# Performance work log

Measured on AMD Instinct MI355X. Metric: run time of the kernel, lower is better.

The kernel has to match this reference:

```python
import jax, jax.numpy as jnp
import numpy as np

B, V = 2048, 64          # batch of polygons, vertices per polygon
D = 2 * V                # data_dim (flattened 2D coords)
HID, TDIM, NL = 256, 128, 4
NH_HID, FPH = 4, 64      # hidden heads, per-head features (hidden_dim//4)
NIN = 2 + 4 + TDIM       # coords + pos_enc(4) + time emb


def _gat_layer(h, src, tgt, W, a_src, a_tgt, b, skip, concat, act, N):
    # gordicaleksa pytorch-GAT GATLayer (imp3), dropout=0
    NH, FOUT = a_src.shape
    proj = (h @ W).reshape(N, NH, FOUT)                       # (N,NH,FOUT)
    s_src = (proj * a_src).sum(-1)                            # (N,NH)
    s_tgt = (proj * a_tgt).sum(-1)
    e = jax.nn.leaky_relu(s_src[src] + s_tgt[tgt], negative_slope=0.2)  # (E,NH)
    m = jax.ops.segment_max(e, tgt, num_segments=N)           # stable segment softmax
    ex = jnp.exp(e - m[tgt])
    denom = jax.ops.segment_sum(ex, tgt, num_segments=N)
    alpha = ex / (denom[tgt] + 1e-16)                         # (E,NH)
    out = jax.ops.segment_sum(proj[src] * alpha[:, :, None], tgt, num_segments=N)
    if skip is None:                                          # FIN == FOUT -> direct residual
        out = out + h[:, None, :]
    else:
        out = out + (h @ skip).reshape(N, NH, FOUT)
    out = out.reshape(N, NH * FOUT) if concat else out.mean(axis=1)
    out = out + b
    return jax.nn.elu(out) if act else out


def _forward(x, t, tW, tb, layers, h1W, h1b, h2W, h2b):
    Bsz, Dd = x.shape
    Vn = Dd // 2
    N = Bsz * Vn
    coords = x.reshape(N, 2)
    graph_index = jnp.repeat(jnp.arange(Bsz), Vn)
    node_index = jnp.tile(jnp.arange(Vn), Bsz)
    # SinusoidalPosEmb(TDIM) + Linear + SiLU
    half = TDIM // 2
    freqs = jnp.exp(-jnp.log(10000.0) * jnp.arange(half, dtype=jnp.float32) / (half - 1))
    te = t.astype(jnp.float32)[:, None] * freqs[None, :]
    temb = jnp.concatenate([jnp.sin(te), jnp.cos(te)], axis=1)
    temb = jax.nn.silu(temb @ tW + tb)
    # cycle positional features
    phase = node_index.astype(jnp.float32) * (2.0 * jnp.pi / Vn)
    pos = jnp.stack([jnp.sin(phase), jnp.cos(phase), jnp.sin(2.0 * phase), jnp.cos(2.0 * phase)], axis=1)
    h = jnp.concatenate([coords, pos, temb[graph_index]], axis=1)  # (N, NIN)
    # cycle edge_index: src=[self,self,self], tgt=[next,prev,self]
    base = graph_index * Vn
    slf = jnp.arange(N)
    nxt = base + jnp.remainder(node_index + 1, Vn)
    prv = base + jnp.remainder(node_index - 1, Vn)
    src = jnp.concatenate([slf, slf, slf])
    tgt = jnp.concatenate([nxt, prv, slf])
    for i, (W, a_s, a_t, b, skip) in enumerate(layers):
        last = (i == len(layers) - 1)
        h = _gat_layer(h, src, tgt, W, a_s, a_t, b, skip, concat=not last, act=not last, N=N)
    h = jax.nn.silu(h @ h1W + h1b)
    noise = h @ h2W + h2b                                     # (N, 2)
    return noise.reshape(Bsz, Dd)


def setup_inputs() -> dict:
    key = jax.random.key(0)
    ks = iter(jax.random.split(key, 48))
    def nrm(shape, s=0.05):
        return (jax.random.normal(next(ks), shape, jnp.float32) * s)
    inp = {}
    inp["x"] = jax.random.normal(next(ks), (B, D), jnp.float32)
    inp["t"] = jax.random.randint(next(ks), (B,), 0, 1000)
    inp["tW"] = nrm((TDIM, TDIM)); inp["tb"] = jnp.zeros((TDIM,), jnp.float32)
    fins = [NIN, NH_HID * FPH, NH_HID * FPH, NH_HID * FPH]
    fouts = [FPH, FPH, FPH, HID]
    nhs = [NH_HID, NH_HID, NH_HID, 1]
    for i in range(NL):
        inp[f"W{i}"] = nrm((fins[i], nhs[i] * fouts[i]))
        inp[f"asrc{i}"] = nrm((nhs[i], fouts[i]))
        inp[f"atgt{i}"] = nrm((nhs[i], fouts[i]))
        inp[f"b{i}"] = jnp.zeros((nhs[i] * fouts[i] if i < NL - 1 else fouts[i],), jnp.float32)
    for i in range(NL - 1):  # last layer: FIN==FOUT -> identity skip
        inp[f"skip{i}"] = nrm((fins[i], nhs[i] * fouts[i]))
    inp["h1W"] = nrm((HID, HID)); inp["h1b"] = jnp.zeros((HID,), jnp.float32)
    inp["h2W"] = nrm((HID, 2)); inp["h2b"] = jnp.zeros((2,), jnp.float32)
    return inp


def reference(x, t, tW, tb,
              W0, asrc0, atgt0, b0, skip0,
              W1, asrc1, atgt1, b1, skip1,
              W2, asrc2, atgt2, b2, skip2,
              W3, asrc3, atgt3, b3,
              h1W, h1b, h2W, h2b):
    layers = [(W0, asrc0, atgt0, b0, skip0),
              (W1, asrc1, atgt1, b1, skip1),
              (W2, asrc2, atgt2, b2, skip2),
              (W3, asrc3, atgt3, b3, None)]
    return _forward(x, t, tW, tb, layers, h1W, h1b, h2W, h2b)
```

## Files before the change

### kernel.cpp

```cpp
#include <hip/hip_runtime.h>
#include <hip/hip_bf16.h>

#define VN    64
#define KPAD  264

typedef __bf16 bf16x8 __attribute__((ext_vector_type(8)));
typedef __bf16 bf16x4 __attribute__((ext_vector_type(4)));
typedef float  f32x4  __attribute__((ext_vector_type(4)));

__device__ __forceinline__ float fexp(float x) { return __expf(x); }
__device__ __forceinline__ float frcp(float x) { return __builtin_amdgcn_rcpf(x); }

#define OFF_W0   0
#define OFF_SK0  40960
#define OFF_W1   81920
#define OFF_SK1  147456
#define OFF_W2   212992
#define OFF_SK2  278528
#define OFF_W3   344064
#define OFF_H1W  409600
#define OFF_SA0  475136
#define OFF_SA1  477696
#define OFF_SA2  481792
#define OFF_SA3  485888
#define OFF_END  489984

__global__ void setup_all(const float* __restrict__ W0s, const float* __restrict__ sk0s,
                          const float* __restrict__ W1s, const float* __restrict__ sk1s,
                          const float* __restrict__ W2s, const float* __restrict__ sk2s,
                          const float* __restrict__ W3s, const float* __restrict__ h1Ws,
                          const float* __restrict__ h2W,
                          const float* __restrict__ as0, const float* __restrict__ at0,
                          const float* __restrict__ as1, const float* __restrict__ at1,
                          const float* __restrict__ as2, const float* __restrict__ at2,
                          const float* __restrict__ as3, const float* __restrict__ at3,
                          const int* __restrict__ t, const float* __restrict__ tW,
                          const float* __restrict__ tb,
                          float* __restrict__ h2wt, float* __restrict__ d_temb,
                          __bf16* __restrict__ wp)
{
  int blk = blockIdx.x, tid = threadIdx.x;
  if (blk < 116) {
    __shared__ float shw[16][257];
    const float* src; int fin, dstoff, s;
    if (blk < 20) {
      if (blk < 10) { src = W0s;  dstoff = OFF_W0;  s = blk; }
      else          { src = sk0s; dstoff = OFF_SK0; s = blk - 10; }
      fin = 134;
    } else {
      int r = (blk - 20) >> 4;
      s = (blk - 20) & 15;
      const float* srcs[6] = {W1s, sk1s, W2s, sk2s, W3s, h1Ws};
      const int    offs[6] = {OFF_W1, OFF_SK1, OFF_W2, OFF_SK2, OFF_W3, OFF_H1W};
      src = srcs[r]; dstoff = offs[r]; fin = 256;
    }
#pragma unroll
    for (int it = 0; it < 16; it++) {
      int elem = it * 256 + tid;
      int r = elem >> 8, n = elem & 255;
      int k = s * 16 + r;
      shw[r][n] = (k < fin) ? src[k * 256 + n] : 0.0f;
    }
    __syncthreads();
#pragma unroll
    for (int it = 0; it < 16; it++) {
      int lin = it * 256 + tid;
      int k7 = lin & 7, n = (lin >> 3) & 255, cl = lin >> 11;
      wp[dstoff + s * 4096 + lin] = (__bf16)shw[cl * 8 + k7][n];
    }
  } else if (blk < 118) {
    int idx = (blk - 116) * 256 + tid;
    int c = idx >> 8, k = idx & 255;
    h2wt[idx] = h2W[k * 2 + c];
  } else if (blk < 176) {
    int idx = (blk - 118) * 256 + tid;
    if (idx < 14848) {
      int gk = idx >> 4, c = idx & 15;
      int li, k, fin, dstoff;
      if (gk < 160)      { li = 0; k = gk;       fin = 134; dstoff = OFF_SA0; }
      else if (gk < 416) { li = 1; k = gk - 160; fin = 256; dstoff = OFF_SA1; }
      else if (gk < 672) { li = 2; k = gk - 416; fin = 256; dstoff = OFF_SA2; }
      else               { li = 3; k = gk - 672; fin = 256; dstoff = OFF_SA3; }
      float v = 0.0f;
      if (k < fin) {
        if (li < 3) {
          if (c < 8) {
            int hd = c & 3;
            const float* Wm = (li == 0) ? W0s : (li == 1) ? W1s : W2s;
            const float* a  = (c < 4) ? ((li == 0) ? as0 : (li == 1) ? as1 : as2)
                                      : ((li == 0) ? at0 : (li == 1) ? at1 : at2);
            for (int f = 0; f < 64; f++)
              v += Wm[k * 256 + hd * 64 + f] * a[hd * 64 + f];
          }
        } else {
          if (c < 2) {
            const float* a = (c == 0) ? as3 : at3;
            for (int f = 0; f < 256; f++)
              v += W3s[k * 256 + f] * a[f];
          }
        }
      }
      wp[dstoff + ((k >> 3) * 16 + c) * 8 + (k & 7)] = (__bf16)v;
    }
  } else {
    __shared__ float se[2][128];
    int half = tid >> 7, tt = tid & 127;
    int b = (blk - 176) * 2 + half;
    int fi = tt & 63;
    float fr = expf(-logf(10000.0f) * (float)fi / 63.0f);
    float te = (float)t[b] * fr;
    se[half][tt] = (tt < 64) ? sinf(te) : cosf(te);
    __syncthreads();
    float a = tb[tt];
    for (int k = 0; k < 128; k++)
      a = fmaf(se[half][k], tW[k * 128 + tt], a);
    d_temb[b * 128 + tt] = a * frcp(1.0f + fexp(-a));
  }
}

template<int KS>
__device__ __forceinline__ void mfma_mm(const __bf16* __restrict__ Bp,
                                        f32x4 acc[4][4],
                                        const __bf16* __restrict__ shA,
                                        int l, int q, int colbase8)
{
#pragma unroll
  for (int s = 0; s < KS; s++) {
    bf16x8 af[4], bfr[4];
#pragma unroll
    for (int rt = 0; rt < 4; rt++)
      af[rt] = *(const bf16x8*)(shA + (rt * 16 + l) * KPAD + s * 32 + q * 8);
#pragma unroll
    for (int ct = 0; ct < 4; ct++)
      bfr[ct] = *(const bf16x8*)(Bp + (s * 4 + q) * 2048 + colbase8 + ct * 128);
#pragma unroll
    for (int rt = 0; rt < 4; rt++)
#pragma unroll
      for (int ct = 0; ct < 4; ct++)
        acc[rt][ct] = __builtin_amdgcn_mfma_f32_16x16x32_bf16(af[rt], bfr[ct], acc[rt][ct], 0, 0, 0);
  }
}

template<int KS>
__device__ __forceinline__ void mfma_mm_sc(const __bf16* __restrict__ Bp,
                                           const __bf16* __restrict__ SAp,
                                           f32x4 acc[4][4], f32x4 acc_sc[4],
                                           const __bf16* __restrict__ shA,
                                           int l, int q, int colbase8)
{
#pragma unroll
  for (int s = 0; s < KS; s++) {
    bf16x8 af[4], bfr[4], bsc;
#pragma unroll
    for (int rt = 0; rt < 4; rt++)
      af[rt] = *(const bf16x8*)(shA + (rt * 16 + l) * KPAD + s * 32 + q * 8);
#pragma unroll
    for (int ct = 0; ct < 4; ct++)
      bfr[ct] = *(const bf16x8*)(Bp + (s * 4 + q) * 2048 + colbase8 + ct * 128);
    bsc = *(const bf16x8*)(SAp + (s * 4 + q) * 128 + l * 8);
#pragma unroll
    for (int rt = 0; rt < 4; rt++) {
#pragma unroll
      for (int ct = 0; ct < 4; ct++)
        acc[rt][ct] = __builtin_amdgcn_mfma_f32_16x16x32_bf16(af[rt], bfr[ct], acc[rt][ct], 0, 0, 0);
      acc_sc[rt] = __builtin_amdgcn_mfma_f32_16x16x32_bf16(af[rt], bsc, acc_sc[rt], 0, 0, 0);
    }
  }
}

__global__ __launch_bounds__(256, 2)
void gat_poly_kernel(const float* __restrict__ x,
                     const float* __restrict__ b0, const float* __restrict__ b1,
                     const float* __restrict__ b2, const float* __restrict__ b3,
                     const float* __restrict__ h1b, const float* __restrict__ h2b,
                     const __bf16* __restrict__ WP,
                     const float* __restrict__ h2wt,
                     const float* __restrict__ d_temb,
                     float* __restrict__ out)
{
  __shared__ __bf16 bufA[VN * KPAD];
  __shared__ __bf16 bufB[VN * KPAD];
  __shared__ float  sh_temb[128];
  __shared__ float  sh_ssp[VN * 4];
  __shared__ float  sh_stp[VN * 4];
  __shared__ float  sh_al[VN][4][3];

  const int b    = blockIdx.x;
  const int tid  = threadIdx.x;
  const int w    = tid >> 6;
  const int lane = tid & 63;
  const int l    = lane & 15;
  const int q    = lane >> 4;
  const int cb   = w * 64;
  const int colbase8 = (cb + l) * 8;

  const int fq  = (tid & 63) * 4;
  const int ns  = (tid >> 6) * 16;
  const int qhd = fq >> 6;

  __bf16* hb = bufA;
  __bf16* ag = bufB;

  if (tid < 128) sh_temb[tid] = d_temb[b * 128 + tid];
  __syncthreads();

  for (int idx = tid; idx < VN * 160; idx += 256) {
    int n = idx / 160, k = idx - n * 160;
    float v = 0.0f;
    if (k < 2) {
      v = x[b * 128 + 2 * n + k];
    } else if (k < 6) {
      float ph  = (float)n * 0.09817477042468103f;
      float arg = (k < 4) ? ph : 2.0f * ph;
      v = ((k & 1) == 0) ? sinf(arg) : cosf(arg);
    } else if (k < 134) {
      v = sh_temb[k - 6];
    }
    hb[n * KPAD + k] = (__bf16)v;
  }
  __syncthreads();

  const int WOFFS[3]  = {OFF_W0, OFF_W1, OFF_W2};
  const int SOFFS[3]  = {OFF_SK0, OFF_SK1, OFF_SK2};
  const int SAOFFS[3] = {OFF_SA0, OFF_SA1, OFF_SA2};
  const float* Bs[3]  = {b0, b1, b2};

  for (int li = 0; li < 3; li++) {
    {
      f32x4 accS[4][4];
#pragma unroll
      for (int rt = 0; rt < 4; rt++)
#pragma unroll
        for (int ct = 0; ct < 4; ct++) accS[rt][ct] = (f32x4)0.0f;
      if (li == 0) mfma_mm<5>(WP + OFF_SK0,   accS, hb, l, q, colbase8);
      else         mfma_mm<8>(WP + SOFFS[li], accS, hb, l, q, colbase8);
      float b4[4];
#pragma unroll
      for (int ct = 0; ct < 4; ct++) b4[ct] = Bs[li][cb + ct * 16 + l];
#pragma unroll
      for (int rt = 0; rt < 4; rt++)
#pragma unroll
        for (int reg = 0; reg < 4; reg++) {
          int n = rt * 16 + q * 4 + reg;
#pragma unroll
          for (int ct = 0; ct < 4; ct++)
            ag[n * KPAD + cb + ct * 16 + l] = (__bf16)(accS[rt][ct][reg] + b4[ct]);
        }
    }

    f32x4 acc[4][4], acc_sc[4];
#pragma unroll
    for (int rt = 0; rt < 4; rt++) {
#pragma unroll
      for (int ct = 0; ct < 4; ct++) acc[rt][ct] = (f32x4)0.0f;
      acc_sc[rt] = (f32x4)0.0f;
    }
    if (li == 0) mfma_mm_sc<5>(WP + OFF_W0,    WP + OFF_SA0,    acc, acc_sc, hb, l, q, colbase8);
    else         mfma_mm_sc<8>(WP + WOFFS[li], WP + SAOFFS[li], acc, acc_sc, hb, l, q, colbase8);

    if (l < 8) {
#pragma unroll
      for (int rt = 0; rt < 4; rt++)
#pragma unroll
        for (int reg = 0; reg < 4; reg++) {
          int n = rt * 16 + q * 4 + reg;
          float v = acc_sc[rt][reg];
          if (l < 4) sh_ssp[n * 4 + l] = v;
          else       sh_stp[n * 4 + (l - 4)] = v;
        }
    }
    __syncthreads();

#pragma unroll
    for (int rt = 0; rt < 4; rt++)
#pragma unroll
      for (int reg = 0; reg < 4; reg++) {
        int n = rt * 16 + q * 4 + reg;
#pragma unroll
        for (int ct = 0; ct < 4; ct++)
          hb[n * KPAD + cb + ct * 16 + l] = (__bf16)acc[rt][ct][reg];
      }

    {
      int n = tid >> 2, hd = tid & 3;
      int prv = (n + 63) & 63, nxt = (n + 1) & 63;
      float stg = sh_stp[n * 4 + hd];
      float e0 = sh_ssp[prv * 4 + hd] + stg; e0 = (e0 < 0.0f) ? 0.2f * e0 : e0;
      float e1 = sh_ssp[nxt * 4 + hd] + stg; e1 = (e1 < 0.0f) ? 0.2f * e1 : e1;
      float e2 = sh_ssp[n * 4 + hd]   + stg; e2 = (e2 < 0.0f) ? 0.2f * e2 : e2;
      float mx = fmaxf(e0, fmaxf(e1, e2));
      float x0 = fexp(e0 - mx), x1 = fexp(e1 - mx), x2 = fexp(e2 - mx);
      float inv = frcp(x0 + x1 + x2 + 1e-16f);
      sh_al[n][hd][0] = x0 * inv;
      sh_al[n][hd][1] = x1 * inv;
      sh_al[n][hd][2] = x2 * inv;
    }
    __syncthreads();

    {
      float pm[4], pc[4];
      { bf16x4 v = *(const bf16x4*)(hb + ((ns + 63) & 63) * KPAD + fq);
#pragma unroll
        for (int j = 0; j < 4; j++) pm[j] = (float)v[j]; }
      { bf16x4 v = *(const bf16x4*)(hb + ns * KPAD + fq);
#pragma unroll
        for (int j = 0; j < 4; j++) pc[j] = (float)v[j]; }
#pragma unroll 4
      for (int i = 0; i < 16; i++) {
        int n = ns + i;
        bf16x4 pnv = *(const bf16x4*)(hb + ((n + 1) & 63) * KPAD + fq);
        bf16x4 agv = *(const bf16x4*)(ag + n * KPAD + fq);
        float a0 = sh_al[n][qhd][0], a1 = sh_al[n][qhd][1], a2 = sh_al[n][qhd][2];
        bf16x4 ov;
#pragma unroll
        for (int j = 0; j < 4; j++) {
          float pn = (float)pnv[j];
          float o = a0 * pm[j] + a1 * pn + a2 * pc[j] + (float)agv[j];
          o = (o > 0.0f) ? o : (fexp(o) - 1.0f);
          ov[j] = (__bf16)o;
          pm[j] = pc[j]; pc[j] = pn;
        }
        *(bf16x4*)(ag + n * KPAD + fq) = ov;
      }
    }
    __syncthreads();

    __bf16* tmp = hb; hb = ag; ag = tmp;
  }

  {
    f32x4 acc[4][4], acc_sc[4];
#pragma unroll
    for (int rt = 0; rt < 4; rt++) {
#pragma unroll
      for (int ct = 0; ct < 4; ct++) acc[rt][ct] = (f32x4)0.0f;
      acc_sc[rt] = (f32x4)0.0f;
    }
    mfma_mm_sc<8>(WP + OFF_W3, WP + OFF_SA3, acc, acc_sc, hb, l, q, colbase8);

    if (l < 2) {
#pragma unroll
      for (int rt = 0; rt < 4; rt++)
#pragma unroll
        for (int reg = 0; reg < 4; reg++) {
          int n = rt * 16 + q * 4 + reg;
          float v = acc_sc[rt][reg];
          if (l == 0) sh_ssp[n * 4] = v;
          else        sh_stp[n * 4] = v;
        }
    }
    __syncthreads();

#pragma unroll
    for (int rt = 0; rt < 4; rt++)
#pragma unroll
      for (int reg = 0; reg < 4; reg++) {
        int n = rt * 16 + q * 4 + reg;
#pragma unroll
        for (int ct = 0; ct < 4; ct++)
          ag[n * KPAD + cb + ct * 16 + l] = (__bf16)acc[rt][ct][reg];
      }

    if (tid < 64) {
      int n = tid;
      float ssn = sh_ssp[n * 4];
      float stn = sh_stp[n * 4];
      float ssp = __shfl(ssn, (n + 63) & 63, 64);
      float ssx = __shfl(ssn, (n + 1) & 63, 64);
      float e0 = ssp + stn; e0 = (e0 < 0.0f) ? 0.2f * e0 : e0;
      float e1 = ssx + stn; e1 = (e1 < 0.0f) ? 0.2f * e1 : e1;
      float e2 = ssn + stn; e2 = (e2 < 0.0f) ? 0.2f * e2 : e2;
      float mx = fmaxf(e0, fmaxf(e1, e2));
      float x0 = fexp(e0 - mx), x1 = fexp(e1 - mx), x2 = fexp(e2 - mx);
      float inv = frcp(x0 + x1 + x2 + 1e-16f);
      sh_al[n][0][0] = x0 * inv;
      sh_al[n][0][1] = x1 * inv;
      sh_al[n][0][2] = x2 * inv;
    }
    __syncthreads();

    {
      float b3r[4];
#pragma unroll
      for (int j = 0; j < 4; j++) b3r[j] = b3[fq + j];
      float pm[4], pc[4];
      { bf16x4 v = *(const bf16x4*)(ag + ((ns + 63) & 63) * KPAD + fq);
#pragma unroll
        for (int j = 0; j < 4; j++) pm[j] = (float)v[j]; }
      { bf16x4 v = *(const bf16x4*)(ag + ns * KPAD + fq);
#pragma unroll
        for (int j = 0; j < 4; j++) pc[j] = (float)v[j]; }
#pragma unroll 4
      for (int i = 0; i < 16; i++) {
        int n = ns + i;
        bf16x4 pnv = *(const bf16x4*)(ag + ((n + 1) & 63) * KPAD + fq);
        bf16x4 hrv = *(const bf16x4*)(hb + n * KPAD + fq);
        float a0 = sh_al[n][0][0], a1 = sh_al[n][0][1], a2 = sh_al[n][0][2];
        bf16x4 ov;
#pragma unroll
        for (int j = 0; j < 4; j++) {
          float pn = (float)pnv[j];
          float o = a0 * pm[j] + a1 * pn + a2 * pc[j] + (float)hrv[j] + b3r[j];
          ov[j] = (__bf16)o;
          pm[j] = pc[j]; pc[j] = pn;
        }
        *(bf16x4*)(hb + n * KPAD + fq) = ov;
      }
    }
    __syncthreads();
  }

  {
    f32x4 acc[4][4];
#pragma unroll
    for (int rt = 0; rt < 4; rt++)
#pragma unroll
      for (int ct = 0; ct < 4; ct++) acc[rt][ct] = (f32x4)0.0f;
    mfma_mm<8>(WP + OFF_H1W, acc, hb, l, q, colbase8);
    __syncthreads();

    float b4[4];
#pragma unroll
    for (int ct = 0; ct < 4; ct++) b4[ct] = h1b[cb + ct * 16 + l];
#pragma unroll
    for (int rt = 0; rt < 4; rt++)
#pragma unroll
      for (int reg = 0; reg < 4; reg++) {
        int n = rt * 16 + q * 4 + reg;
#pragma unroll
        for (int ct = 0; ct < 4; ct++) {
          float o = acc[rt][ct][reg] + b4[ct];
          o = o * frcp(1.0f + fexp(-o));
          hb[n * KPAD + cb + ct * 16 + l] = (__bf16)o;
        }
      }
    __syncthreads();

    {
      int n = tid >> 2, c = (tid >> 1) & 1, half = tid & 1;
      const float* wrow = h2wt + c * 256 + half * 128;
      const __bf16* hrow = hb + n * KPAD + half * 128;
      float o = half ? 0.0f : h2b[c];
#pragma unroll 4
      for (int k8 = 0; k8 < 16; k8++) {
        bf16x8 hv = *(const bf16x8*)(hrow + k8 * 8);
        f32x4 w0 = *(const f32x4*)(wrow + k8 * 8);
        f32x4 w1 = *(const f32x4*)(wrow + k8 * 8 + 4);
#pragma unroll
        for (int j = 0; j < 4; j++) o = fmaf((float)hv[j], w0[j], o);
#pragma unroll
        for (int j = 0; j < 4; j++) o = fmaf((float)hv[4 + j], w1[j], o);
      }
      o += __shfl_xor(o, 1, 64);
      if (!half) out[b * 128 + 2 * n + c] = o;
    }
  }
}

extern "C" void kernel_launch(void* const* d_in, const int* in_sizes, int n_in,
                              void* d_out, int out_size, void* d_ws, size_t ws_size,
                              hipStream_t stream)
{
  auto fp = [&](int i) { return (const float*)d_in[i]; };
  __bf16* wp   = (__bf16*)d_ws;
  float* h2wt  = (float*)(wp + OFF_END);
  float* dtemb = h2wt + 512;

  setup_all<<<1200, 256, 0, stream>>>(fp(4), fp(20), fp(8), fp(21),
                                      fp(12), fp(22), fp(16), fp(23),
                                      fp(25),
                                      fp(5),  fp(6),  fp(9),  fp(10),
                                      fp(13), fp(14), fp(17), fp(18),
                                      (const int*)d_in[1], fp(2), fp(3),
                                      h2wt, dtemb, wp);

  gat_poly_kernel<<<2048, 256, 0, stream>>>(
      fp(0),
      fp(7), fp(11), fp(15), fp(19),
      fp(24), fp(26),
      wp, h2wt, dtemb,
      (float*)d_out);
}
```

Measured before the change: 368.5 us.

## Permute weight columns so MFMA epilogue writes contiguous bf16x4 and widen aggregation to bf16x8

The setup kernel permutes output columns of the packed weights so that each lane's four MFMA column tiles land on four adjacent features. The epilogue can then store one bf16x4 vector per row instead of four scalar bf16 LDS writes. The neighbour-aggregation loops are also reorganised to have each thread handle 8 features across 8 nodes using bf16x8 LDS loads and stores. This cuts LDS instruction count and may reduce bank conflicts, at the cost of more registers held per thread in the aggregation loop.

```diff
diff --git a/kernel.cpp b/kernel.cpp
--- a/kernel.cpp
+++ b/kernel.cpp
@@ -24,6 +24,10 @@
 #define OFF_SA2  481792
 #define OFF_SA3  485888
 #define OFF_END  489984
+
+__device__ __forceinline__ int permcol(int n) {
+  return (n & 0xC0) | (((n & 15) << 2) | ((n >> 4) & 3));
+}
 
 __global__ void setup_all(const float* __restrict__ W0s, const float* __restrict__ sk0s,
                           const float* __restrict__ W1s, const float* __restrict__ sk1s,
@@ -66,7 +70,7 @@
     for (int it = 0; it < 16; it++) {
       int lin = it * 256 + tid;
       int k7 = lin & 7, n = (lin >> 3) & 255, cl = lin >> 11;
-      wp[dstoff + s * 4096 + lin] = (__bf16)shw[cl * 8 + k7][n];
+      wp[dstoff + s * 4096 + lin] = (__bf16)shw[cl * 8 + k7][permcol(n)];
     }
   } else if (blk < 118) {
     int idx = (blk - 116) * 256 + tid;
@@ -193,10 +197,11 @@
   const int q    = lane >> 4;
   const int cb   = w * 64;
   const int colbase8 = (cb + l) * 8;
-
-  const int fq  = (tid & 63) * 4;
-  const int ns  = (tid >> 6) * 16;
-  const int qhd = fq >> 6;
+  const int fb   = cb + 4 * l;
+
+  const int fo  = (tid & 31) * 8;
+  const int no  = (tid >> 5) * 8;
+  const int ohd = fo >> 6;
 
   __bf16* hb = bufA;
   __bf16* ag = bufB;
@@ -236,15 +241,16 @@
       else         mfma_mm<8>(WP + SOFFS[li], accS, hb, l, q, colbase8);
       float b4[4];
 #pragma unroll
-      for (int ct = 0; ct < 4; ct++) b4[ct] = Bs[li][cb + ct * 16 + l];
+      for (int ct = 0; ct < 4; ct++) b4[ct] = Bs[li][fb + ct];
 #pragma unroll
       for (int rt = 0; rt < 4; rt++)
 #pragma unroll
         for (int reg = 0; reg < 4; reg++) {
           int n = rt * 16 + q * 4 + reg;
-#pragma unroll
-          for (int ct = 0; ct < 4; ct++)
-            ag[n * KPAD + cb + ct * 16 + l] = (__bf16)(accS[rt][ct][reg] + b4[ct]);
+          bf16x4 ov;
+#pragma unroll
+          for (int ct = 0; ct < 4; ct++) ov[ct] = (__bf16)(accS[rt][ct][reg] + b4[ct]);
+          *(bf16x4*)(ag + n * KPAD + fb) = ov;
         }
     }
 
@@ -276,9 +282,10 @@
 #pragma unroll
       for (int reg = 0; reg < 4; reg++) {
         int n = rt * 16 + q * 4 + reg;
-#pragma unroll
-        for (int ct = 0; ct < 4; ct++)
-          hb[n * KPAD + cb + ct * 16 + l] = (__bf16)acc[rt][ct][reg];
+        bf16x4 ov;
+#pragma unroll
+        for (int ct = 0; ct < 4; ct++) ov[ct] = (__bf16)acc[rt][ct][reg];
+        *(bf16x4*)(hb + n * KPAD + fb) = ov;
       }
 
     {
@@ -298,29 +305,29 @@
     __syncthreads();
 
     {
-      float pm[4], pc[4];
-      { bf16x4 v = *(const bf16x4*)(hb + ((ns + 63) & 63) * KPAD + fq);
-#pragma unroll
-        for (int j = 0; j < 4; j++) pm[j] = (float)v[j]; }
-      { bf16x4 v = *(const bf16x4*)(hb + ns * KPAD + fq);
-#pragma unroll
-        for (int j = 0; j < 4; j++) pc[j] = (float)v[j]; }
-#pragma unroll 4
-      for (int i = 0; i < 16; i++) {
-        int n = ns + i;
-        bf16x4 pnv = *(const bf16x4*)(hb + ((n + 1) & 63) * KPAD + fq);
-        bf16x4 agv = *(const bf16x4*)(ag + n * KPAD + fq);
-        float a0 = sh_al[n][qhd][0], a1 = sh_al[n][qhd][1], a2 = sh_al[n][qhd][2];
-        bf16x4 ov;
-#pragma unroll
-        for (int j = 0; j < 4; j++) {
+      float pm[8], pc[8];
+      { bf16x8 v = *(const bf16x8*)(hb + ((no + 63) & 63) * KPAD + fo);
+#pragma unroll
+        for (int j = 0; j < 8; j++) pm[j] = (float)v[j]; }
+      { bf16x8 v = *(const bf16x8*)(hb + no * KPAD + fo);
+#pragma unroll
+        for (int j = 0; j < 8; j++) pc[j] = (float)v[j]; }
+#pragma unroll
+      for (int i = 0; i < 8; i++) {
+        int n = no + i;
+        bf16x8 pnv = *(const bf16x8*)(hb + ((n + 1) & 63) * KPAD + fo);
+        bf16x8 agv = *(const bf16x8*)(ag + n * KPAD + fo);
+        float a0 = sh_al[n][ohd][0], a1 = sh_al[n][ohd][1], a2 = sh_al[n][ohd][2];
+        bf16x8 ov;
+#pragma unroll
+        for (int j = 0; j < 8; j++) {
           float pn = (float)pnv[j];
           float o = a0 * pm[j] + a1 * pn + a2 * pc[j] + (float)agv[j];
           o = (o > 0.0f) ? o : (fexp(o) - 1.0f);
           ov[j] = (__bf16)o;
           pm[j] = pc[j]; pc[j] = pn;
         }
-        *(bf16x4*)(ag + n * KPAD + fq) = ov;
+        *(bf16x8*)(ag + n * KPAD + fo) = ov;
       }
     }
     __syncthreads();
@@ -356,9 +363,10 @@
 #pragma unroll
       for (int reg = 0; reg < 4; reg++) {
         int n = rt * 16 + q * 4 + reg;
-#pragma unroll
-        for (int ct = 0; ct < 4; ct++)
-          ag[n * KPAD + cb + ct * 16 + l] = (__bf16)acc[rt][ct][reg];
+        bf16x4 ov;
+#pragma unroll
+        for (int ct = 0; ct < 4; ct++) ov[ct] = (__bf16)acc[rt][ct][reg];
+        *(bf16x4*)(ag + n * KPAD + fb) = ov;
       }
 
     if (tid < 64) {
@@ -380,31 +388,31 @@
     __syncthreads();
 
     {
-      float b3r[4];
-#pragma unroll
-      for (int j = 0; j < 4; j++) b3r[j] = b3[fq + j];
-      float pm[4], pc[4];
-      { bf16x4 v = *(const bf16x4*)(ag + ((ns + 63) & 63) * KPAD + fq);
-#pragma unroll
-        for (int j = 0; j < 4; j++) pm[j] = (float)v[j]; }
-      { bf16x4 v = *(const bf16x4*)(ag + ns * KPAD + fq);
-#pragma unroll
-        for (int j = 0; j < 4; j++) pc[j] = (float)v[j]; }
-#pragma unroll 4
-      for (int i = 0; i < 16; i++) {
-        int n = ns + i;
-        bf16x4 pnv = *(const bf16x4*)(ag + ((n + 1) & 63) * KPAD + fq);
-        bf16x4 hrv = *(const bf16x4*)(hb + n * KPAD + fq);
+      float b3r[8];
+#pragma unroll
+      for (int j = 0; j < 8; j++) b3r[j] = b3[fo + j];
+      float pm[8], pc[8];
+      { bf16x8 v = *(const bf16x8*)(ag + ((no + 63) & 63) * KPAD + fo);
+#pragma unroll
+        for (int j = 0; j < 8; j++) pm[j] = (float)v[j]; }
+      { bf16x8 v = *(const bf16x8*)(ag + no * KPAD + fo);
+#pragma unroll
+        for (int j = 0; j < 8; j++) pc[j] = (float)v[j]; }
+#pragma unroll
+      for (int i = 0; i < 8; i++) {
+        int n = no + i;
+        bf16x8 pnv = *(const bf16x8*)(ag + ((n + 1) & 63) * KPAD + fo);
+        bf16x8 hrv = *(const bf16x8*)(hb + n * KPAD + fo);
         float a0 = sh_al[n][0][0], a1 = sh_al[n][0][1], a2 = sh_al[n][0][2];
-        bf16x4 ov;
-#pragma unroll
-        for (int j = 0; j < 4; j++) {
+        bf16x8 ov;
+#pragma unroll
+        for (int j = 0; j < 8; j++) {
           float pn = (float)pnv[j];
           float o = a0 * pm[j] + a1 * pn + a2 * pc[j] + (float)hrv[j] + b3r[j];
           ov[j] = (__bf16)o;
           pm[j] = pc[j]; pc[j] = pn;
         }
-        *(bf16x4*)(hb + n * KPAD + fq) = ov;
+        *(bf16x8*)(hb + n * KPAD + fo) = ov;
       }
     }
     __syncthreads();
@@ -421,18 +429,20 @@
 
     float b4[4];
 #pragma unroll
-    for (int ct = 0; ct < 4; ct++) b4[ct] = h1b[cb + ct * 16 + l];
+    for (int ct = 0; ct < 4; ct++) b4[ct] = h1b[fb + ct];
 #pragma unroll
     for (int rt = 0; rt < 4; rt++)
 #pragma unroll
       for (int reg = 0; reg < 4; reg++) {
         int n = rt * 16 + q * 4 + reg;
+        bf16x4 ov;
 #pragma unroll
         for (int ct = 0; ct < 4; ct++) {
           float o = acc[rt][ct][reg] + b4[ct];
           o = o * frcp(1.0f + fexp(-o));
-          hb[n * KPAD + cb + ct * 16 + l] = (__bf16)o;
-        }
+          ov[ct] = (__bf16)o;
+        }
+        *(bf16x4*)(hb + n * KPAD + fb) = ov;
       }
     __syncthreads();
 
```

Result: faster. 357.5 us (-3.0%).
